# Optimization experiments

Measured on AMD Instinct MI355X. Metric: run time of the kernel, lower is better.

Reference implementation:

```python
import jax, jax.numpy as jnp
import numpy as np

N, P, C, HID, H, W = 100000, 8, 256, 256, 512, 512
RADIUS = 2.0
D = C + 2


def setup_inputs() -> dict:
    key = jax.random.key(0)
    ks = jax.random.split(key, 9)
    return {
        "guided_queries": jax.random.normal(ks[0], (N, C), jnp.float32),
        "projection_coords": jax.random.uniform(ks[1], (N, 2), jnp.float32)
        * jnp.array([W - 1.0, H - 1.0], jnp.float32),
        "feature_map": jax.random.normal(ks[2], (H, W, C), jnp.float32),
        "off_ln_g": jnp.ones((D,), jnp.float32),
        "off_ln_b": jnp.zeros((D,), jnp.float32),
        "off_W1": jax.random.normal(ks[3], (D, HID), jnp.float32) * 0.05,
        "off_b1": jnp.zeros((HID,), jnp.float32),
        "off_W2": jax.random.normal(ks[4], (HID, HID), jnp.float32) * 0.05,
        "off_b2": jnp.zeros((HID,), jnp.float32),
        "off_W3": jax.random.normal(ks[5], (HID, P * 2), jnp.float32) * 0.01,
        "off_b3": jnp.zeros((P * 2,), jnp.float32),
        "wgt_ln_g": jnp.ones((D,), jnp.float32),
        "wgt_ln_b": jnp.zeros((D,), jnp.float32),
        "wgt_W1": jax.random.normal(ks[6], (D, HID), jnp.float32) * 0.05,
        "wgt_b1": jnp.zeros((HID,), jnp.float32),
        "wgt_W2": jax.random.normal(ks[7], (HID, HID), jnp.float32) * 0.05,
        "wgt_b2": jnp.zeros((HID,), jnp.float32),
        "wgt_W3": jax.random.normal(ks[8], (HID, P), jnp.float32) * 0.01,
        "wgt_b3": jnp.full((P,), 0.1, jnp.float32),
    }


def _layernorm(x, g, b, eps=1e-5):
    mu = x.mean(-1, keepdims=True)
    var = ((x - mu) ** 2).mean(-1, keepdims=True)
    return (x - mu) * jax.lax.rsqrt(var + eps) * g + b


def _mlp(x, W1, b1, W2, b2, W3, b3):
    # dropout is identity in eval mode
    h = jax.nn.relu(x @ W1 + b1)
    h = jax.nn.relu(h @ W2 + b2)
    return h @ W3 + b3


def _bilinear_border(fmap, coords):
    """fmap (H,W,C); coords (N,P,2) in pixel space -> (N,P,C).
    Matches F.grid_sample(mode='bilinear', padding_mode='border', align_corners=True)
    after the module's normalize + clamp(-1.1, 1.1)."""
    gx = jnp.clip(2.0 * coords[..., 0] / (W - 1) - 1.0, -1.1, 1.1)
    gy = jnp.clip(2.0 * coords[..., 1] / (H - 1) - 1.0, -1.1, 1.1)
    ix = jnp.clip((gx + 1.0) * 0.5 * (W - 1), 0.0, W - 1.0)  # border clamp
    iy = jnp.clip((gy + 1.0) * 0.5 * (H - 1), 0.0, H - 1.0)
    x0 = jnp.floor(ix)
    y0 = jnp.floor(iy)
    wx = (ix - x0)[..., None]
    wy = (iy - y0)[..., None]
    x0i = x0.astype(jnp.int32)
    y0i = y0.astype(jnp.int32)
    x1i = jnp.minimum(x0i + 1, W - 1)
    y1i = jnp.minimum(y0i + 1, H - 1)
    flat = fmap.reshape(H * W, C)
    v00 = flat[y0i * W + x0i]  # (N,P,C)
    v01 = flat[y0i * W + x1i]
    v10 = flat[y1i * W + x0i]
    v11 = flat[y1i * W + x1i]
    return (v00 * (1 - wx) + v01 * wx) * (1 - wy) + (v10 * (1 - wx) + v11 * wx) * wy


def reference(guided_queries, projection_coords, feature_map,
              off_ln_g, off_ln_b, off_W1, off_b1, off_W2, off_b2, off_W3, off_b3,
              wgt_ln_g, wgt_ln_b, wgt_W1, wgt_b1, wgt_W2, wgt_b2, wgt_W3, wgt_b3):
    x = jnp.concatenate([guided_queries, projection_coords], axis=-1)  # (N, C+2)
    off_raw = _mlp(_layernorm(x, off_ln_g, off_ln_b),
                   off_W1, off_b1, off_W2, off_b2, off_W3, off_b3)
    offsets = jnp.tanh(off_raw.reshape(-1, P, 2)) * RADIUS  # (N,P,2)
    wgt_raw = _mlp(_layernorm(x, wgt_ln_g, wgt_ln_b),
                   wgt_W1, wgt_b1, wgt_W2, wgt_b2, wgt_W3, wgt_b3)
    weights = jax.nn.softmax(wgt_raw, axis=-1)  # (N,P)
    coords = projection_coords[:, None, :] + offsets  # (N,P,2)
    sampled = _bilinear_border(feature_map, coords)  # (N,P,C)
    wsum = jnp.clip(weights.sum(-1, keepdims=True), 1e-8, None)
    nw = weights / wsum
    return jnp.sum(nw[..., None] * sampled, axis=1)  # (N,C)
```

## Files before the change

### kernel.cpp

```cpp
#include <hip/hip_runtime.h>

#define NQ   100000
#define PP   8
#define CC   256
#define HIDN 256
#define HH   512
#define WW   512
#define DD   258
#define KK1  288
#define KK2  256
#define TQ   32
#define NTHR 512
#define XS_STRIDE 296

typedef __attribute__((ext_vector_type(8))) __bf16 bf16x8;
typedef __attribute__((ext_vector_type(4))) float  f32x4;
typedef __attribute__((ext_vector_type(4))) unsigned short u16x4;
typedef __attribute__((ext_vector_type(8))) unsigned short u16x8;

__device__ __forceinline__ unsigned short f2bf_hi(float v, float* rem) {
    __bf16 h = (__bf16)v;
    *rem = v - (float)h;
    return __builtin_bit_cast(unsigned short, h);
}
__device__ __forceinline__ unsigned short f2bf(float v) {
    __bf16 h = (__bf16)v;
    return __builtin_bit_cast(unsigned short, h);
}
__device__ __forceinline__ float bf2f(unsigned short h) {
    unsigned int u = ((unsigned int)h) << 16;
    return __builtin_bit_cast(float, u);
}

#define WS_W1TH 0
#define WS_W1TL 294912
#define WS_W2TH 589824
#define WS_W2TL 851968
#define WS_W3T  1114112
#define WS_B1E  1138688

__global__ void prep_w1(const float* __restrict__ og, const float* __restrict__ obl,
                        const float* __restrict__ oW1, const float* __restrict__ ob1,
                        const float* __restrict__ wg, const float* __restrict__ wbl,
                        const float* __restrict__ wW1, const float* __restrict__ wb1,
                        unsigned short* __restrict__ w1th, unsigned short* __restrict__ w1tl,
                        float* __restrict__ b1e) {
    const int br = blockIdx.y, k = blockIdx.x, n = threadIdx.x;
    const float* g  = br ? wg  : og;
    const float* bl = br ? wbl : obl;
    const float* W1 = br ? wW1 : oW1;
    const float* b1 = br ? wb1 : ob1;
    float v = (k < DD) ? g[k] * W1[k * HIDN + n] : 0.f;
    float rem; unsigned short hi = f2bf_hi(v, &rem);
    size_t o = (size_t)br * 256 * KK1 + (size_t)n * KK1 + k;
    w1th[o] = hi; w1tl[o] = f2bf(rem);
    if (k == 0) {
        float s = b1[n];
        for (int kk = 0; kk < DD; ++kk) s += bl[kk] * W1[kk * HIDN + n];
        b1e[br * 256 + n] = s;
    }
}

__global__ void prep_w2(const float* __restrict__ oW2, const float* __restrict__ wW2,
                        unsigned short* __restrict__ w2th, unsigned short* __restrict__ w2tl) {
    const int br = blockIdx.y, k = blockIdx.x, n = threadIdx.x;
    const float* W2 = br ? wW2 : oW2;
    float v = W2[k * HIDN + n];
    float rem; unsigned short hi = f2bf_hi(v, &rem);
    size_t o = (size_t)br * 256 * KK2 + (size_t)n * KK2 + k;
    w2th[o] = hi; w2tl[o] = f2bf(rem);
}

__global__ void prep_w3(const float* __restrict__ oW3, const float* __restrict__ wW3,
                        float* __restrict__ w3t) {
    const int br = blockIdx.x, t = threadIdx.x;
    if (br == 0) {
        const int c = t & 15, kb = t >> 4;
        for (int i = 0; i < 16; ++i) { int k = kb * 16 + i; w3t[c * 256 + k] = oW3[k * 16 + c]; }
    } else {
        const int c = t & 7, kb = t >> 3;
        for (int i = 0; i < 8; ++i)  { int k = kb * 8 + i;  w3t[(16 + c) * 256 + k] = wW3[k * 8 + c]; }
    }
}

__launch_bounds__(NTHR, 4)
__global__ void fused_kernel(const float* __restrict__ gq, const float* __restrict__ pc,
                             const float* __restrict__ fmap,
                             const unsigned short* __restrict__ w1th, const unsigned short* __restrict__ w1tl,
                             const unsigned short* __restrict__ w2th, const unsigned short* __restrict__ w2tl,
                             const float* __restrict__ w3t, const float* __restrict__ b1e,
                             const float* __restrict__ ob2, const float* __restrict__ ob3,
                             const float* __restrict__ wb2, const float* __restrict__ wb3,
                             float* __restrict__ out) {
    __shared__ __align__(16) unsigned short xsh[TQ * XS_STRIDE];
    __shared__ __align__(16) unsigned short xsl[TQ * XS_STRIDE];
    __shared__ __align__(16) float raw[TQ * 24];
    __shared__ __align__(16) float pcs[TQ * 2];

    const int t    = threadIdx.x;
    const int q0   = blockIdx.x * TQ;
    const int lane = t & 63;
    const int wv   = t >> 6;
    const int quad = lane >> 4;
    const int l15  = lane & 15;

    for (int i = t; i < TQ * XS_STRIDE / 2; i += NTHR) {
        ((unsigned int*)xsh)[i] = 0u; ((unsigned int*)xsl)[i] = 0u;
    }
    if (t < TQ * 2) pcs[t] = pc[(size_t)q0 * 2 + t];
    __syncthreads();

    const float4* gq4 = (const float4*)gq;

    for (int br = 0; br < 2; ++br) {
        #pragma unroll
        for (int qq = 0; qq < 4; ++qq) {
            const int q = wv * 4 + qq;
            const float4 v = gq4[(size_t)(q0 + q) * 64 + lane];
            const float px = pcs[q * 2 + 0], py = pcs[q * 2 + 1];
            float s  = v.x + v.y + v.z + v.w;
            float ss = v.x * v.x + v.y * v.y + v.z * v.z + v.w * v.w;
            if (lane == 0) { s += px + py; ss += px * px + py * py; }
            #pragma unroll
            for (int off = 32; off > 0; off >>= 1) {
                s += __shfl_xor(s, off, 64); ss += __shfl_xor(ss, off, 64);
            }
            const float mu = s * (1.f / DD);
            const float var = fmaxf(ss * (1.f / DD) - mu * mu, 0.f);
            const float rs = rsqrtf(var + 1e-5f);
            const float n0 = (v.x - mu) * rs, n1 = (v.y - mu) * rs;
            const float n2 = (v.z - mu) * rs, n3 = (v.w - mu) * rs;
            float r0, r1, r2, r3;
            u16x4 hh; u16x4 ll;
            hh[0] = f2bf_hi(n0, &r0); hh[1] = f2bf_hi(n1, &r1);
            hh[2] = f2bf_hi(n2, &r2); hh[3] = f2bf_hi(n3, &r3);
            ll[0] = f2bf(r0); ll[1] = f2bf(r1); ll[2] = f2bf(r2); ll[3] = f2bf(r3);
            *(u16x4*)(&xsh[q * XS_STRIDE + lane * 4]) = hh;
            *(u16x4*)(&xsl[q * XS_STRIDE + lane * 4]) = ll;
            if (lane == 0) {
                const float nx = (px - mu) * rs, ny = (py - mu) * rs;
                float rx, ry;
                xsh[q * XS_STRIDE + 256] = f2bf_hi(nx, &rx);
                xsh[q * XS_STRIDE + 257] = f2bf_hi(ny, &ry);
                xsl[q * XS_STRIDE + 256] = f2bf(rx);
                xsl[q * XS_STRIDE + 257] = f2bf(ry);
            }
        }
        __syncthreads();

        {
            f32x4 acc[2][2];
            #pragma unroll
            for (int mt = 0; mt < 2; ++mt)
                #pragma unroll
                for (int nt = 0; nt < 2; ++nt) {
                    float b = b1e[br * 256 + wv * 32 + nt * 16 + l15];
                    acc[mt][nt] = (f32x4){b, b, b, b};
                }
            const unsigned short* Wh = w1th + (size_t)br * 256 * KK1;
            const unsigned short* Wl = w1tl + (size_t)br * 256 * KK1;
            const unsigned short* a0h = xsh + l15 * XS_STRIDE + quad * 8;
            const unsigned short* a0l = xsl + l15 * XS_STRIDE + quad * 8;
            const unsigned short* a1h = a0h + 16 * XS_STRIDE;
            const unsigned short* a1l = a0l + 16 * XS_STRIDE;
            for (int k0 = 0; k0 < KK1; k0 += 32) {
                const bf16x8 ah0 = *(const bf16x8*)(a0h + k0);
                const bf16x8 al0 = *(const bf16x8*)(a0l + k0);
                const bf16x8 ah1 = *(const bf16x8*)(a1h + k0);
                const bf16x8 al1 = *(const bf16x8*)(a1l + k0);
                #pragma unroll
                for (int nt = 0; nt < 2; ++nt) {
                    const size_t n = wv * 32 + nt * 16 + l15;
                    const bf16x8 bh = *(const bf16x8*)(Wh + n * KK1 + k0 + quad * 8);
                    const bf16x8 bl = *(const bf16x8*)(Wl + n * KK1 + k0 + quad * 8);
                    acc[0][nt] = __builtin_amdgcn_mfma_f32_16x16x32_bf16(ah0, bh, acc[0][nt], 0, 0, 0);
                    acc[0][nt] = __builtin_amdgcn_mfma_f32_16x16x32_bf16(ah0, bl, acc[0][nt], 0, 0, 0);
                    acc[0][nt] = __builtin_amdgcn_mfma_f32_16x16x32_bf16(al0, bh, acc[0][nt], 0, 0, 0);
                    acc[1][nt] = __builtin_amdgcn_mfma_f32_16x16x32_bf16(ah1, bh, acc[1][nt], 0, 0, 0);
                    acc[1][nt] = __builtin_amdgcn_mfma_f32_16x16x32_bf16(ah1, bl, acc[1][nt], 0, 0, 0);
                    acc[1][nt] = __builtin_amdgcn_mfma_f32_16x16x32_bf16(al1, bh, acc[1][nt], 0, 0, 0);
                }
            }
            __syncthreads();
            #pragma unroll
            for (int mt = 0; mt < 2; ++mt)
                #pragma unroll
                for (int nt = 0; nt < 2; ++nt) {
                    const int n = wv * 32 + nt * 16 + l15;
                    #pragma unroll
                    for (int r = 0; r < 4; ++r) {
                        const int m = mt * 16 + quad * 4 + r;
                        float v = fmaxf(acc[mt][nt][r], 0.f);
                        float rem;
                        xsh[m * XS_STRIDE + n] = f2bf_hi(v, &rem);
                        xsl[m * XS_STRIDE + n] = f2bf(rem);
                    }
                }
        }
        __syncthreads();

        {
            const float* b2 = br ? wb2 : ob2;
            f32x4 acc[2][2];
            #pragma unroll
            for (int mt = 0; mt < 2; ++mt)
                #pragma unroll
                for (int nt = 0; nt < 2; ++nt) {
                    float b = b2[wv * 32 + nt * 16 + l15];
                    acc[mt][nt] = (f32x4){b, b, b, b};
                }
            const unsigned short* Wh = w2th + (size_t)br * 256 * KK2;
            const unsigned short* Wl = w2tl + (size_t)br * 256 * KK2;
            const unsigned short* a0h = xsh + l15 * XS_STRIDE + quad * 8;
            const unsigned short* a0l = xsl + l15 * XS_STRIDE + quad * 8;
            const unsigned short* a1h = a0h + 16 * XS_STRIDE;
            const unsigned short* a1l = a0l + 16 * XS_STRIDE;
            for (int k0 = 0; k0 < KK2; k0 += 32) {
                const bf16x8 ah0 = *(const bf16x8*)(a0h + k0);
                const bf16x8 al0 = *(const bf16x8*)(a0l + k0);
                const bf16x8 ah1 = *(const bf16x8*)(a1h + k0);
                const bf16x8 al1 = *(const bf16x8*)(a1l + k0);
                #pragma unroll
                for (int nt = 0; nt < 2; ++nt) {
                    const size_t n = wv * 32 + nt * 16 + l15;
                    const bf16x8 bh = *(const bf16x8*)(Wh + n * KK2 + k0 + quad * 8);
                    const bf16x8 bl = *(const bf16x8*)(Wl + n * KK2 + k0 + quad * 8);
                    acc[0][nt] = __builtin_amdgcn_mfma_f32_16x16x32_bf16(ah0, bh, acc[0][nt], 0, 0, 0);
                    acc[0][nt] = __builtin_amdgcn_mfma_f32_16x16x32_bf16(ah0, bl, acc[0][nt], 0, 0, 0);
                    acc[0][nt] = __builtin_amdgcn_mfma_f32_16x16x32_bf16(al0, bh, acc[0][nt], 0, 0, 0);
                    acc[1][nt] = __builtin_amdgcn_mfma_f32_16x16x32_bf16(ah1, bh, acc[1][nt], 0, 0, 0);
                    acc[1][nt] = __builtin_amdgcn_mfma_f32_16x16x32_bf16(ah1, bl, acc[1][nt], 0, 0, 0);
                    acc[1][nt] = __builtin_amdgcn_mfma_f32_16x16x32_bf16(al1, bh, acc[1][nt], 0, 0, 0);
                }
            }
            __syncthreads();
            #pragma unroll
            for (int mt = 0; mt < 2; ++mt)
                #pragma unroll
                for (int nt = 0; nt < 2; ++nt) {
                    const int n = wv * 32 + nt * 16 + l15;
                    #pragma unroll
                    for (int r = 0; r < 4; ++r) {
                        const int m = mt * 16 + quad * 4 + r;
                        float v = fmaxf(acc[mt][nt][r], 0.f);
                        float rem;
                        xsh[m * XS_STRIDE + n] = f2bf_hi(v, &rem);
                        xsl[m * XS_STRIDE + n] = f2bf(rem);
                    }
                }
        }
        __syncthreads();

        if (br == 0) {
            const int q = t >> 4, c = t & 15;
            float s = ob3[c];
            const float4* w4 = (const float4*)(w3t + c * 256);
            const unsigned short* hrow = xsh + q * XS_STRIDE;
            const unsigned short* lrow = xsl + q * XS_STRIDE;
            for (int k = 0; k < 256; k += 8) {
                const u16x8 hi = *(const u16x8*)(hrow + k);
                const u16x8 lo = *(const u16x8*)(lrow + k);
                const float4 wa = w4[(k >> 2)];
                const float4 wb = w4[(k >> 2) + 1];
                s += (bf2f(hi[0]) + bf2f(lo[0])) * wa.x + (bf2f(hi[1]) + bf2f(lo[1])) * wa.y
                   + (bf2f(hi[2]) + bf2f(lo[2])) * wa.z + (bf2f(hi[3]) + bf2f(lo[3])) * wa.w
                   + (bf2f(hi[4]) + bf2f(lo[4])) * wb.x + (bf2f(hi[5]) + bf2f(lo[5])) * wb.y
                   + (bf2f(hi[6]) + bf2f(lo[6])) * wb.z + (bf2f(hi[7]) + bf2f(lo[7])) * wb.w;
            }
            raw[q * 24 + c] = s;
        } else if (t < TQ * 8) {
            const int q = t >> 3, c = t & 7;
            float s = wb3[c];
            const float4* w4 = (const float4*)(w3t + (16 + c) * 256);
            const unsigned short* hrow = xsh + q * XS_STRIDE;
            const unsigned short* lrow = xsl + q * XS_STRIDE;
            for (int k = 0; k < 256; k += 8) {
                const u16x8 hi = *(const u16x8*)(hrow + k);
                const u16x8 lo = *(const u16x8*)(lrow + k);
                const float4 wa = w4[(k >> 2)];
                const float4 wb = w4[(k >> 2) + 1];
                s += (bf2f(hi[0]) + bf2f(lo[0])) * wa.x + (bf2f(hi[1]) + bf2f(lo[1])) * wa.y
                   + (bf2f(hi[2]) + bf2f(lo[2])) * wa.z + (bf2f(hi[3]) + bf2f(lo[3])) * wa.w
                   + (bf2f(hi[4]) + bf2f(lo[4])) * wb.x + (bf2f(hi[5]) + bf2f(lo[5])) * wb.y
                   + (bf2f(hi[6]) + bf2f(lo[6])) * wb.z + (bf2f(hi[7]) + bf2f(lo[7])) * wb.w;
            }
            raw[q * 24 + 16 + c] = s;
        }
        __syncthreads();
    }

    int*   sidx = (int*)xsh;
    float* sw   = (float*)xsl;
    if (t < TQ) {
        const int q = t;
        float m = -1e30f;
        #pragma unroll
        for (int p = 0; p < 8; ++p) m = fmaxf(m, raw[q * 24 + 16 + p]);
        float e[8]; float S = 0.f;
        #pragma unroll
        for (int p = 0; p < 8; ++p) { e[p] = expf(raw[q * 24 + 16 + p] - m); S += e[p]; }
        float s2 = 0.f;
        #pragma unroll
        for (int p = 0; p < 8; ++p) { e[p] /= S; s2 += e[p]; }
        const float inv = 1.f / fmaxf(s2, 1e-8f);

        const float px = pcs[q * 2 + 0], py = pcs[q * 2 + 1];
        #pragma unroll
        for (int p = 0; p < 8; ++p) {
            const float cx = px + 2.f * tanhf(raw[q * 24 + 2 * p]);
            const float cy = py + 2.f * tanhf(raw[q * 24 + 2 * p + 1]);
            const float gx = fminf(fmaxf(2.f * cx * (1.f / (WW - 1)) - 1.f, -1.1f), 1.1f);
            const float gy = fminf(fmaxf(2.f * cy * (1.f / (HH - 1)) - 1.f, -1.1f), 1.1f);
            const float ix = fminf(fmaxf((gx + 1.f) * 0.5f * (WW - 1), 0.f), (float)(WW - 1));
            const float iy = fminf(fmaxf((gy + 1.f) * 0.5f * (HH - 1), 0.f), (float)(HH - 1));
            const float x0 = floorf(ix), y0 = floorf(iy);
            const float wx = ix - x0, wy = iy - y0;
            const int x0i = (int)x0, y0i = (int)y0;
            const int x1i = min(x0i + 1, WW - 1), y1i = min(y0i + 1, HH - 1);
            const float nwp = e[p] * inv;
            const int b = (q * 8 + p) * 4;
            sidx[b + 0] = (y0i * WW + x0i) * (CC / 4);
            sidx[b + 1] = (y0i * WW + x1i) * (CC / 4);
            sidx[b + 2] = (y1i * WW + x0i) * (CC / 4);
            sidx[b + 3] = (y1i * WW + x1i) * (CC / 4);
            sw[b + 0] = (1.f - wx) * (1.f - wy) * nwp;
            sw[b + 1] = wx * (1.f - wy) * nwp;
            sw[b + 2] = (1.f - wx) * wy * nwp;
            sw[b + 3] = wx * wy * nwp;
        }
    }
    __syncthreads();

    const float4* fm4 = (const float4*)fmap;
    float4* out4 = (float4*)out;
    #pragma unroll
    for (int qq = 0; qq < 4; ++qq) {
        const int q = wv * 4 + qq;
        float4 acc; acc.x = acc.y = acc.z = acc.w = 0.f;
        for (int p = 0; p < 8; ++p) {
            const int b = (q * 8 + p) * 4;
            const int i00 = sidx[b + 0] + lane;
            const int i01 = sidx[b + 1] + lane;
            const int i10 = sidx[b + 2] + lane;
            const int i11 = sidx[b + 3] + lane;
            const float a00 = sw[b + 0], a01 = sw[b + 1], a10 = sw[b + 2], a11 = sw[b + 3];
            const float4 v00 = fm4[i00], v01 = fm4[i01], v10 = fm4[i10], v11 = fm4[i11];
            acc.x += a00 * v00.x + a01 * v01.x + a10 * v10.x + a11 * v11.x;
            acc.y += a00 * v00.y + a01 * v01.y + a10 * v10.y + a11 * v11.y;
            acc.z += a00 * v00.z + a01 * v01.z + a10 * v10.z + a11 * v11.z;
            acc.w += a00 * v00.w + a01 * v01.w + a10 * v10.w + a11 * v11.w;
        }
        out4[(size_t)(q0 + q) * (CC / 4) + lane] = acc;
    }
}

extern "C" void kernel_launch(void* const* d_in, const int* in_sizes, int n_in,
                              void* d_out, int out_size, void* d_ws, size_t ws_size,
                              hipStream_t stream) {
    const float* gq   = (const float*)d_in[0];
    const float* pc   = (const float*)d_in[1];
    const float* fmap = (const float*)d_in[2];
    const float* og   = (const float*)d_in[3];
    const float* obl  = (const float*)d_in[4];
    const float* oW1  = (const float*)d_in[5];
    const float* ob1  = (const float*)d_in[6];
    const float* oW2  = (const float*)d_in[7];
    const float* ob2  = (const float*)d_in[8];
    const float* oW3  = (const float*)d_in[9];
    const float* ob3  = (const float*)d_in[10];
    const float* wg   = (const float*)d_in[11];
    const float* wbl  = (const float*)d_in[12];
    const float* wW1  = (const float*)d_in[13];
    const float* wb1  = (const float*)d_in[14];
    const float* wW2  = (const float*)d_in[15];
    const float* wb2  = (const float*)d_in[16];
    const float* wW3  = (const float*)d_in[17];
    const float* wb3  = (const float*)d_in[18];

    char* ws = (char*)d_ws;
    unsigned short* w1th = (unsigned short*)(ws + WS_W1TH);
    unsigned short* w1tl = (unsigned short*)(ws + WS_W1TL);
    unsigned short* w2th = (unsigned short*)(ws + WS_W2TH);
    unsigned short* w2tl = (unsigned short*)(ws + WS_W2TL);
    float* w3t = (float*)(ws + WS_W3T);
    float* b1e = (float*)(ws + WS_B1E);
    float* out = (float*)d_out;

    prep_w1<<<dim3(KK1, 2), 256, 0, stream>>>(og, obl, oW1, ob1, wg, wbl, wW1, wb1, w1th, w1tl, b1e);
    prep_w2<<<dim3(KK2, 2), 256, 0, stream>>>(oW2, wW2, w2th, w2tl);
    prep_w3<<<2, 256, 0, stream>>>(oW3, wW3, w3t);
    fused_kernel<<<NQ / TQ, NTHR, 0, stream>>>(gq, pc, fmap, w1th, w1tl, w2th, w2tl, w3t, b1e,
                                               ob2, ob3, wb2, wb3, out);
}
```

Baseline: 1.197 ms.

## Split fused MLP+gather kernel into separate MLP and bilinear-gather kernels

The fused kernel is split in two. The MLP kernel now writes per-sample records (cell index, fractional weights, normalized weight) to workspace, and a new lightweight gather kernel with small blocks performs the bilinear gather and weighted sum. This decouples the latency-bound gather from the heavy MLP block's occupancy limits, at the cost of an extra launch and a global round trip for the sample records. The bias-folding loop in prep_w1 is also unrolled into four accumulators.

Result: no change. 1.217 ms (+1.6%).

```diff
diff --git a/kernel.cpp b/kernel.cpp
--- a/kernel.cpp
+++ b/kernel.cpp
@@ -12,6 +12,7 @@
 #define TQ   32
 #define NTHR 512
 #define XS_STRIDE 296
+#define GQB  4
 
 typedef __attribute__((ext_vector_type(8))) __bf16 bf16x8;
 typedef __attribute__((ext_vector_type(4))) float  f32x4;
@@ -38,6 +39,7 @@
 #define WS_W2TL 851968
 #define WS_W3T  1114112
 #define WS_B1E  1138688
+#define WS_SP   1140736
 
 __global__ void prep_w1(const float* __restrict__ og, const float* __restrict__ obl,
                         const float* __restrict__ oW1, const float* __restrict__ ob1,
@@ -55,8 +57,15 @@
     size_t o = (size_t)br * 256 * KK1 + (size_t)n * KK1 + k;
     w1th[o] = hi; w1tl[o] = f2bf(rem);
     if (k == 0) {
-        float s = b1[n];
-        for (int kk = 0; kk < DD; ++kk) s += bl[kk] * W1[kk * HIDN + n];
+        float a0 = 0.f, a1 = 0.f, a2 = 0.f, a3 = 0.f;
+        for (int kk = 0; kk < 256; kk += 4) {
+            a0 += bl[kk + 0] * W1[(kk + 0) * HIDN + n];
+            a1 += bl[kk + 1] * W1[(kk + 1) * HIDN + n];
+            a2 += bl[kk + 2] * W1[(kk + 2) * HIDN + n];
+            a3 += bl[kk + 3] * W1[(kk + 3) * HIDN + n];
+        }
+        float s = b1[n] + a0 + a1 + a2 + a3
+                + bl[256] * W1[256 * HIDN + n] + bl[257] * W1[257 * HIDN + n];
         b1e[br * 256 + n] = s;
     }
 }
@@ -84,14 +93,13 @@
 }
 
 __launch_bounds__(NTHR, 4)
-__global__ void fused_kernel(const float* __restrict__ gq, const float* __restrict__ pc,
-                             const float* __restrict__ fmap,
-                             const unsigned short* __restrict__ w1th, const unsigned short* __restrict__ w1tl,
-                             const unsigned short* __restrict__ w2th, const unsigned short* __restrict__ w2tl,
-                             const float* __restrict__ w3t, const float* __restrict__ b1e,
-                             const float* __restrict__ ob2, const float* __restrict__ ob3,
-                             const float* __restrict__ wb2, const float* __restrict__ wb3,
-                             float* __restrict__ out) {
+__global__ void mlp_kernel(const float* __restrict__ gq, const float* __restrict__ pc,
+                           const unsigned short* __restrict__ w1th, const unsigned short* __restrict__ w1tl,
+                           const unsigned short* __restrict__ w2th, const unsigned short* __restrict__ w2tl,
+                           const float* __restrict__ w3t, const float* __restrict__ b1e,
+                           const float* __restrict__ ob2, const float* __restrict__ ob3,
+                           const float* __restrict__ wb2, const float* __restrict__ wb3,
+                           float4* __restrict__ sp) {
     __shared__ __align__(16) unsigned short xsh[TQ * XS_STRIDE];
     __shared__ __align__(16) unsigned short xsl[TQ * XS_STRIDE];
     __shared__ __align__(16) float raw[TQ * 24];
@@ -289,8 +297,6 @@
         __syncthreads();
     }
 
-    int*   sidx = (int*)xsh;
-    float* sw   = (float*)xsl;
     if (t < TQ) {
         const int q = t;
         float m = -1e30f;
@@ -315,43 +321,51 @@
             const float iy = fminf(fmaxf((gy + 1.f) * 0.5f * (HH - 1), 0.f), (float)(HH - 1));
             const float x0 = floorf(ix), y0 = floorf(iy);
             const float wx = ix - x0, wy = iy - y0;
-            const int x0i = (int)x0, y0i = (int)y0;
-            const int x1i = min(x0i + 1, WW - 1), y1i = min(y0i + 1, HH - 1);
-            const float nwp = e[p] * inv;
-            const int b = (q * 8 + p) * 4;
-            sidx[b + 0] = (y0i * WW + x0i) * (CC / 4);
-            sidx[b + 1] = (y0i * WW + x1i) * (CC / 4);
-            sidx[b + 2] = (y1i * WW + x0i) * (CC / 4);
-            sidx[b + 3] = (y1i * WW + x1i) * (CC / 4);
-            sw[b + 0] = (1.f - wx) * (1.f - wy) * nwp;
-            sw[b + 1] = wx * (1.f - wy) * nwp;
-            sw[b + 2] = (1.f - wx) * wy * nwp;
-            sw[b + 3] = wx * wy * nwp;
-        }
-    }
+            const int cell = (int)y0 * WW + (int)x0;
+            float4 rec;
+            rec.x = __int_as_float(cell);
+            rec.y = wx; rec.z = wy; rec.w = e[p] * inv;
+            sp[(size_t)(q0 + q) * 8 + p] = rec;
+        }
+    }
+}
+
+__launch_bounds__(256, 8)
+__global__ void gather_kernel(const float* __restrict__ fmap,
+                              const float4* __restrict__ sp,
+                              float* __restrict__ out) {
+    __shared__ float4 spb[GQB * 8];
+    const int t    = threadIdx.x;
+    const int q0   = blockIdx.x * GQB;
+    const int lane = t & 63;
+    const int wv   = t >> 6;
+
+    if (t < GQB * 8) spb[t] = sp[(size_t)q0 * 8 + t];
     __syncthreads();
 
     const float4* fm4 = (const float4*)fmap;
-    float4* out4 = (float4*)out;
-    #pragma unroll
-    for (int qq = 0; qq < 4; ++qq) {
-        const int q = wv * 4 + qq;
-        float4 acc; acc.x = acc.y = acc.z = acc.w = 0.f;
-        for (int p = 0; p < 8; ++p) {
-            const int b = (q * 8 + p) * 4;
-            const int i00 = sidx[b + 0] + lane;
-            const int i01 = sidx[b + 1] + lane;
-            const int i10 = sidx[b + 2] + lane;
-            const int i11 = sidx[b + 3] + lane;
-            const float a00 = sw[b + 0], a01 = sw[b + 1], a10 = sw[b + 2], a11 = sw[b + 3];
-            const float4 v00 = fm4[i00], v01 = fm4[i01], v10 = fm4[i10], v11 = fm4[i11];
-            acc.x += a00 * v00.x + a01 * v01.x + a10 * v10.x + a11 * v11.x;
-            acc.y += a00 * v00.y + a01 * v01.y + a10 * v10.y + a11 * v11.y;
-            acc.z += a00 * v00.z + a01 * v01.z + a10 * v10.z + a11 * v11.z;
-            acc.w += a00 * v00.w + a01 * v01.w + a10 * v10.w + a11 * v11.w;
-        }
-        out4[(size_t)(q0 + q) * (CC / 4) + lane] = acc;
-    }
+    float4 acc; acc.x = acc.y = acc.z = acc.w = 0.f;
+    for (int p = 0; p < 8; ++p) {
+        const float4 d = spb[wv * 8 + p];
+        const int cell = __float_as_int(d.x);
+        const int x0 = cell & (WW - 1), y0 = cell >> 9;
+        const int x1 = min(x0 + 1, WW - 1), y1 = min(y0 + 1, HH - 1);
+        const float wx = d.y, wy = d.z, nwp = d.w;
+        const float w00 = (1.f - wx) * (1.f - wy) * nwp;
+        const float w01 = wx * (1.f - wy) * nwp;
+        const float w10 = (1.f - wx) * wy * nwp;
+        const float w11 = wx * wy * nwp;
+        const int b00 = (y0 * WW + x0) * (CC / 4) + lane;
+        const int b01 = (y0 * WW + x1) * (CC / 4) + lane;
+        const int b10 = (y1 * WW + x0) * (CC / 4) + lane;
+        const int b11 = (y1 * WW + x1) * (CC / 4) + lane;
+        const float4 v00 = fm4[b00], v01 = fm4[b01], v10 = fm4[b10], v11 = fm4[b11];
+        acc.x += w00 * v00.x + w01 * v01.x + w10 * v10.x + w11 * v11.x;
+        acc.y += w00 * v00.y + w01 * v01.y + w10 * v10.y + w11 * v11.y;
+        acc.z += w00 * v00.z + w01 * v01.z + w10 * v10.z + w11 * v11.z;
+        acc.w += w00 * v00.w + w01 * v01.w + w10 * v10.w + w11 * v11.w;
+    }
+    ((float4*)out)[(size_t)(q0 + wv) * (CC / 4) + lane] = acc;
 }
 
 extern "C" void kernel_launch(void* const* d_in, const int* in_sizes, int n_in,
@@ -384,11 +398,13 @@
     unsigned short* w2tl = (unsigned short*)(ws + WS_W2TL);
     float* w3t = (float*)(ws + WS_W3T);
     float* b1e = (float*)(ws + WS_B1E);
+    float4* sp = (float4*)(ws + WS_SP);
     float* out = (float*)d_out;
 
     prep_w1<<<dim3(KK1, 2), 256, 0, stream>>>(og, obl, oW1, ob1, wg, wbl, wW1, wb1, w1th, w1tl, b1e);
     prep_w2<<<dim3(KK2, 2), 256, 0, stream>>>(oW2, wW2, w2th, w2tl);
     prep_w3<<<2, 256, 0, stream>>>(oW3, wW3, w3t);
-    fused_kernel<<<NQ / TQ, NTHR, 0, stream>>>(gq, pc, fmap, w1th, w1tl, w2th, w2tl, w3t, b1e,
-                                               ob2, ob3, wb2, wb3, out);
-}
+    mlp_kernel<<<NQ / TQ, NTHR, 0, stream>>>(gq, pc, w1th, w1tl, w2th, w2tl, w3t, b1e,
+                                             ob2, ob3, wb2, wb3, sp);
+    gather_kernel<<<NQ / GQB, 256, 0, stream>>>(fmap, sp, out);
+}
```
